# Optimization experiments

Hardware: AMD Instinct MI355X
Metric: run time of the kernel (lower is better)

## Reference

```python
import jax, jax.numpy as jnp
import numpy as np

B, E, N, NREL, K, T, L = 8, 2000, 10000, 25, 16, 3, 32
TAU1 = 10.0

def _clip01(x):
    return jnp.clip(x, 0.0, 1.0)

def setup_inputs():
    key = jax.random.key(0)
    ks = jax.random.split(key, 10)
    ent = jax.random.randint(ks[0], (B,), 0, E)
    input_x = jnp.zeros((B, E), jnp.float32).at[jnp.arange(B), ent].set(1.0)
    tidx = jax.random.randint(ks[1], (E,), 0, K)
    type_mat = jnp.zeros((E, K), jnp.float32).at[jnp.arange(E), tidx].set(1.0)
    heads = jax.random.randint(ks[2], (N,), 0, E)
    tails = jax.random.randint(ks[3], (N,), 0, E)
    rels = jax.random.randint(ks[4], (N,), 0, NREL)
    e2triple = jnp.zeros((E, N), jnp.float32).at[heads, jnp.arange(N)].set(1.0)
    triple2e = jnp.zeros((N, E), jnp.float32).at[jnp.arange(N), tails].set(1.0)
    triple2r = jnp.zeros((N, NREL), jnp.float32).at[jnp.arange(N), rels].set(1.0)
    def ku(k, shape):
        fan_in = int(np.prod(shape[1:]))
        bnd = 1.0 / np.sqrt(fan_in)
        return jax.random.uniform(k, shape, jnp.float32, -bnd, bnd)
    w = ku(ks[5], (T, L, NREL))
    weight = ku(ks[6], (L, 1))
    h = jnp.ones((T, L, NREL - 1), jnp.float32)
    h_x = jnp.ones((L, NREL - 1), jnp.float32)
    h_type = ku(ks[7], (T, L, K))
    h_x_type = ku(ks[8], (L, K))
    alpha = jnp.ones((T, L), jnp.float32)
    beta = jnp.ones((T, L), jnp.float32)
    alpha_x = jnp.ones((L,), jnp.float32)
    beta_x = jnp.ones((L,), jnp.float32)
    return dict(input_x=input_x, type_mat=type_mat, e2triple=e2triple,
                triple2e=triple2e, triple2r=triple2r, w=w, weight=weight,
                h=h, h_x=h_x, h_type=h_type, h_x_type=h_x_type,
                alpha=alpha, beta=beta, alpha_x=alpha_x, beta_x=beta_x, flag=0)

def _forward(input_x, type_mat, e2triple, triple2e, triple2r, w, weight,
             h, h_x, h_type, h_x_type, alpha, beta, alpha_x, beta_x):
    # flag=False, is_training=False path of TCLMModel.forward
    Bb = input_x.shape[0]
    Nn, Ee = triple2e.shape
    Tt, Ll = alpha.shape
    nrel = w.shape[-1]
    half = (nrel - 1) // 2
    x_ori = input_x @ e2triple                      # [B,N]
    e2r = triple2e.T @ triple2r                     # [E,nrel]
    hidden_base = _clip01(e2r)[:, :-1]              # [E,nrel-1]
    hx_raw = _clip01(x_ori @ triple2r)              # [B,nrel]
    hidden_x_base = jnp.concatenate([hx_raw[:, half:-1], hx_raw[:, :half]], axis=-1)
    ax = _clip01(alpha_x / TAU1)
    bx = _clip01(beta_x / TAU1)
    gate_x = 1.0 - _clip01(ax + bx)                 # [L]
    hxp = _clip01(h_x / TAU1)                       # [L,nrel-1]
    hxtp = _clip01(h_x_type / TAU1)                 # [L,K]
    hidden_type_x = input_x @ (type_mat @ hxtp.T)   # [B,L]
    hx_lin = hidden_x_base @ hxp.T                  # [B,L]
    s = None
    for t in range(Tt):
        a = _clip01(alpha[t] / TAU1)                # [L]
        b = _clip01(beta[t] / TAU1)
        hp = _clip01(h[t] / TAU1)                   # [L,nrel-1]
        htp = _clip01(h_type[t] / TAU1)             # [L,K]
        hidden = _clip01(a[None] * (type_mat @ htp.T) + b[None] * (hidden_base @ hp.T))
        hidden = (hidden + (1.0 - _clip01(a + b))[None]).T        # [L,E]
        # note: original code uses alpha/beta (not alpha_x/beta_x) here; replicate
        hidden_x = _clip01(a[None] * hidden_type_x + b[None] * hx_lin) + gate_x[None]  # [B,L]
        w_probs = jax.nn.softmax(w[t], axis=-1)     # [L,nrel]
        srel = triple2r @ w_probs.T                 # [N,L]
        if t == 0:
            sc = x_ori[:, None, :] * srel.T[None]   # [B,L,N]
            s = (sc.reshape(-1, Nn) @ triple2e).reshape(Bb, Ll, Ee)
            s = s * hidden[None] * hidden_x[:, :, None]
        else:
            xprev = (s.reshape(-1, Ee) @ e2triple).reshape(Bb, Ll, Nn)
            sc = xprev * srel.T[None]               # [B,L,N]
            s = (sc.reshape(-1, Nn) @ triple2e).reshape(Bb, Ll, Ee)
            s = s * hidden[None]
    out = jnp.einsum('ble,lk->bek', s, jnp.tanh(weight))[..., 0]  # [B,E]
    return out

def reference(input_x, type_mat, e2triple, triple2e, triple2r, w, weight,
              h, h_x, h_type, h_x_type, alpha, beta, alpha_x, beta_x, flag):
    return _forward(input_x, type_mat, e2triple, triple2e, triple2r, w, weight,
                    h, h_x, h_type, h_x_type, alpha, beta, alpha_x, beta_x)
```

## Files before the change

### kernel.cpp

```cpp
#include <hip/hip_runtime.h>

#define B 8
#define E 2000
#define NTRI 10000
#define NRELS 25
#define KT 16
#define TT 3
#define LL 32
#define TAU1 10.0f
#define XBLK 8192
#define XTHR 256

typedef __attribute__((ext_vector_type(4))) float f32x4;

__device__ __forceinline__ float clip01(float x) { return fminf(fmaxf(x, 0.0f), 1.0f); }

__global__ void __launch_bounds__(XTHR) extract_all(
        const f32x4* __restrict__ e2t, const f32x4* __restrict__ t2e,
        const float4* __restrict__ t2r, const float4* __restrict__ ix,
        const float4* __restrict__ tm,
        int* __restrict__ heads, int* __restrict__ tails, int* __restrict__ rels,
        int* __restrict__ ent, int* __restrict__ tidx, float4* __restrict__ out4) {
    const int gtid = blockIdx.x * XTHR + threadIdx.x;
    const int gs = XBLK * XTHR;

    for (int i = gtid; i < B * E / 4; i += gs) {
        float4 v = ix[i];
        if (v.x != 0.f || v.y != 0.f || v.z != 0.f || v.w != 0.f) {
            int f = i * 4;
            float c[4] = {v.x, v.y, v.z, v.w};
#pragma unroll
            for (int k = 0; k < 4; k++)
                if (c[k] != 0.f) { int a = f + k; int b = a / E; ent[b] = a - b * E; }
        }
    }
    for (int i = gtid; i < E * KT / 4; i += gs) {
        float4 v = tm[i];
        if (v.x != 0.f || v.y != 0.f || v.z != 0.f || v.w != 0.f) {
            int f = i * 4;
            float c[4] = {v.x, v.y, v.z, v.w};
#pragma unroll
            for (int k = 0; k < 4; k++)
                if (c[k] != 0.f) { int a = f + k; int e = a / KT; tidx[e] = a - e * KT; }
        }
    }
    float4 z = make_float4(0.f, 0.f, 0.f, 0.f);
    for (int i = gtid; i < B * E / 4; i += gs) out4[i] = z;

    for (int i = gtid; i < NTRI * NRELS / 4; i += gs) {
        float4 v = t2r[i];
        if (v.x != 0.f || v.y != 0.f || v.z != 0.f || v.w != 0.f) {
            int f = i * 4;
            float c[4] = {v.x, v.y, v.z, v.w};
#pragma unroll
            for (int k = 0; k < 4; k++)
                if (c[k] != 0.f) {
                    int a = f + k;
                    int j = a / NRELS;
                    rels[j] = a - j * NRELS;
                }
        }
    }
    for (int i = gtid; i < E * NTRI / 4; i += gs) {
        f32x4 v = __builtin_nontemporal_load(&e2t[i]);
        if (v.x != 0.f || v.y != 0.f || v.z != 0.f || v.w != 0.f) {
            int f = i * 4;
            float c[4] = {v.x, v.y, v.z, v.w};
#pragma unroll
            for (int k = 0; k < 4; k++)
                if (c[k] != 0.f) {
                    int a = f + k;
                    int head = a / NTRI;
                    heads[a - head * NTRI] = head;
                }
        }
    }
    for (int i = gtid; i < NTRI * E / 4; i += gs) {
        f32x4 v = __builtin_nontemporal_load(&t2e[i]);
        if (v.x != 0.f || v.y != 0.f || v.z != 0.f || v.w != 0.f) {
            int f = i * 4;
            float c[4] = {v.x, v.y, v.z, v.w};
#pragma unroll
            for (int k = 0; k < 4; k++)
                if (c[k] != 0.f) {
                    int a = f + k;
                    int j = a / E;
                    tails[j] = a - j * E;
                }
        }
    }
}

__global__ void __launch_bounds__(512) mega_prop(
        const int* __restrict__ heads, const int* __restrict__ tails,
        const int* __restrict__ rels, const int* __restrict__ ent,
        const int* __restrict__ tidx,
        const float* __restrict__ w, const float* __restrict__ h,
        const float* __restrict__ h_type, const float* __restrict__ alpha,
        const float* __restrict__ beta, const float* __restrict__ h_x,
        const float* __restrict__ h_x_type, const float* __restrict__ alpha_x,
        const float* __restrict__ beta_x, const float* __restrict__ weight,
        float* __restrict__ out) {
    __shared__ float prev[E];
    __shared__ float acc[E];
    __shared__ unsigned int mask_s[E];
    __shared__ int tidx_s[E];
    __shared__ float wrow[NRELS];
    __shared__ float hp[NRELS - 1];
    __shared__ float htpL[KT];
    __shared__ unsigned int relflag;
    __shared__ float extra_s;

    const int NT = 512;
    const int blk = blockIdx.x, b = blk >> 5, l = blk & 31, tid = threadIdx.x;
    const int ent_b = ent[b];

    for (int e = tid; e < E; e += NT) {
        acc[e] = 0.f;
        mask_s[e] = 0u;
        tidx_s[e] = tidx[e];
    }
    if (tid == 0) { relflag = 0u; extra_s = 1.f; }

    const uint4* h4 = (const uint4*)heads;
    const uint4* t4 = (const uint4*)tails;
    const uint4* r4 = (const uint4*)rels;

    for (int t = 0; t < TT; t++) {
        const int tl = t * LL + l;
        if (tid == 0) {
            const float* wr = w + tl * NRELS;
            float mx = wr[0];
            for (int r = 1; r < NRELS; r++) mx = fmaxf(mx, wr[r]);
            float ex[NRELS], s = 0.f;
            for (int r = 0; r < NRELS; r++) { ex[r] = expf(wr[r] - mx); s += ex[r]; }
            float inv = 1.f / s;
            for (int r = 0; r < NRELS; r++) wrow[r] = ex[r] * inv;
        }
        if (tid >= 64 && tid < 64 + NRELS - 1)
            hp[tid - 64] = clip01(h[tl * (NRELS - 1) + (tid - 64)] / TAU1);
        if (tid >= 128 && tid < 128 + KT)
            htpL[tid - 128] = clip01(h_type[tl * KT + (tid - 128)] / TAU1);
        __syncthreads();

        if (t == 0) {
            for (int i = tid; i < NTRI / 4; i += NT) {
                uint4 hh = h4[i], ttv = t4[i], rr = r4[i];
#pragma unroll
                for (int k = 0; k < 4; k++) {
                    unsigned int hd = (k == 0) ? hh.x : (k == 1) ? hh.y : (k == 2) ? hh.z : hh.w;
                    unsigned int ta = (k == 0) ? ttv.x : (k == 1) ? ttv.y : (k == 2) ? ttv.z : ttv.w;
                    unsigned int r  = (k == 0) ? rr.x : (k == 1) ? rr.y : (k == 2) ? rr.z : rr.w;
                    if (r < NRELS - 1) atomicOr(&mask_s[ta], 1u << r);
                    if ((int)hd == ent_b) {
                        atomicAdd(&acc[ta], wrow[r]);
                        atomicOr(&relflag, 1u << r);
                    }
                }
            }
        } else {
            for (int i = tid; i < NTRI / 4; i += NT) {
                uint4 hh = h4[i], ttv = t4[i], rr = r4[i];
#pragma unroll
                for (int k = 0; k < 4; k++) {
                    unsigned int hd = (k == 0) ? hh.x : (k == 1) ? hh.y : (k == 2) ? hh.z : hh.w;
                    float pv = prev[hd];
                    if (pv != 0.f) {
                        unsigned int ta = (k == 0) ? ttv.x : (k == 1) ? ttv.y : (k == 2) ? ttv.z : ttv.w;
                        unsigned int r  = (k == 0) ? rr.x : (k == 1) ? rr.y : (k == 2) ? rr.z : rr.w;
                        atomicAdd(&acc[ta], pv * wrow[r]);
                    }
                }
            }
        }
        __syncthreads();

        const float a = clip01(alpha[tl] / TAU1);
        const float bb = clip01(beta[tl] / TAU1);
        const float base = 1.f - clip01(a + bb);

        if (t == 0 && tid == 0) {
            unsigned int fl = relflag;
            float hxlin = 0.f;
            for (int i = 0; i < NRELS - 1; i++) {
                int pi = (i < 12) ? (12 + i) : (i - 12);
                if ((fl >> pi) & 1u) hxlin += clip01(h_x[l * (NRELS - 1) + i] / TAU1);
            }
            float htx = clip01(h_x_type[l * KT + tidx_s[ent_b]] / TAU1);
            float ax = clip01(alpha_x[l] / TAU1), bx = clip01(beta_x[l] / TAU1);
            extra_s = clip01(a * htx + bb * hxlin) + (1.f - clip01(ax + bx));
        }
        __syncthreads();

        const float extra = (t == 0) ? extra_s : 1.f;

        if (t < TT - 1) {
            for (int e = tid; e < E; e += NT) {
                unsigned int m = mask_s[e];
                float dot = 0.f;
#pragma unroll
                for (int i = 0; i < NRELS - 1; i++) dot += ((m >> i) & 1u) ? hp[i] : 0.f;
                float he = clip01(a * htpL[tidx_s[e]] + bb * dot) + base;
                prev[e] = acc[e] * he * extra;
                acc[e] = 0.f;
            }
        } else {
            float tw = tanhf(weight[l]);
            for (int e = tid; e < E; e += NT) {
                unsigned int m = mask_s[e];
                float dot = 0.f;
#pragma unroll
                for (int i = 0; i < NRELS - 1; i++) dot += ((m >> i) & 1u) ? hp[i] : 0.f;
                float he = clip01(a * htpL[tidx_s[e]] + bb * dot) + base;
                atomicAdd(&out[b * E + e], acc[e] * he * tw);
            }
        }
        __syncthreads();
    }
}

extern "C" void kernel_launch(void* const* d_in, const int* in_sizes, int n_in,
                              void* d_out, int out_size, void* d_ws, size_t ws_size,
                              hipStream_t stream) {
    const float* input_x  = (const float*)d_in[0];
    const float* type_mat = (const float*)d_in[1];
    const float* e2triple = (const float*)d_in[2];
    const float* triple2e = (const float*)d_in[3];
    const float* triple2r = (const float*)d_in[4];
    const float* w        = (const float*)d_in[5];
    const float* weight   = (const float*)d_in[6];
    const float* h        = (const float*)d_in[7];
    const float* h_x      = (const float*)d_in[8];
    const float* h_type   = (const float*)d_in[9];
    const float* h_x_type = (const float*)d_in[10];
    const float* alpha    = (const float*)d_in[11];
    const float* beta     = (const float*)d_in[12];
    const float* alpha_x  = (const float*)d_in[13];
    const float* beta_x   = (const float*)d_in[14];
    (void)in_sizes; (void)n_in; (void)out_size; (void)ws_size;

    char* ws = (char*)d_ws;
    int* heads = (int*)ws;
    int* tails = heads + ((NTRI + 63) & ~63);
    int* rels  = tails + ((NTRI + 63) & ~63);
    int* ent   = rels + ((NTRI + 63) & ~63);
    int* tidx  = ent + 64;

    extract_all<<<XBLK, XTHR, 0, stream>>>((const f32x4*)e2triple, (const f32x4*)triple2e,
                                           (const float4*)triple2r, (const float4*)input_x,
                                           (const float4*)type_mat,
                                           heads, tails, rels, ent, tidx, (float4*)d_out);

    mega_prop<<<B * LL, 512, 0, stream>>>(heads, tails, rels, ent, tidx, w, h, h_type,
                                          alpha, beta, h_x, h_x_type, alpha_x, beta_x,
                                          weight, (float*)d_out);
}
```

Measured before the change: 213.6 us.

## Precompute per-entity relation masks and per-batch head lists in a separate kernel

Adds a build_aux kernel that computes the per-tail relation bitmask once globally and, per batch, a compact list of triples whose head is the query entity. The propagation kernel's first hop now walks only that short list instead of all triples, and the softmax of w moves into the extraction kernel. The extraction kernel also merges the two large dense-matrix scans into one loop, and later hops skip loading tails and relations when all four heads are inactive. The cost is one extra launch, and the lists are capped at LCAP entries, which would silently drop triples if a head had more than that.

```diff
diff --git a/kernel.cpp b/kernel.cpp
--- a/kernel.cpp
+++ b/kernel.cpp
@@ -10,6 +10,7 @@
 #define TAU1 10.0f
 #define XBLK 8192
 #define XTHR 256
+#define LCAP 256
 
 typedef __attribute__((ext_vector_type(4))) float f32x4;
 
@@ -18,75 +19,89 @@
 __global__ void __launch_bounds__(XTHR) extract_all(
         const f32x4* __restrict__ e2t, const f32x4* __restrict__ t2e,
         const float4* __restrict__ t2r, const float4* __restrict__ ix,
-        const float4* __restrict__ tm,
+        const float4* __restrict__ tm, const float* __restrict__ w,
         int* __restrict__ heads, int* __restrict__ tails, int* __restrict__ rels,
-        int* __restrict__ ent, int* __restrict__ tidx, float4* __restrict__ out4) {
+        int* __restrict__ ent, int* __restrict__ tidx,
+        unsigned int* __restrict__ mask_g, int* __restrict__ cnt_g,
+        float* __restrict__ wrow_g, float4* __restrict__ out4) {
     const int gtid = blockIdx.x * XTHR + threadIdx.x;
     const int gs = XBLK * XTHR;
+
+    if (gtid < 2048) mask_g[gtid] = 0u;
+    if (gtid < 64) cnt_g[gtid] = 0;
+    float4 z = make_float4(0.f, 0.f, 0.f, 0.f);
+    for (int i = gtid; i < B * E / 4; i += gs) out4[i] = z;
+
+    if (gtid < TT * LL) {
+        const float* wr = w + gtid * NRELS;
+        float mx = wr[0];
+        for (int r = 1; r < NRELS; r++) mx = fmaxf(mx, wr[r]);
+        float ex[NRELS], s = 0.f;
+        for (int r = 0; r < NRELS; r++) { ex[r] = expf(wr[r] - mx); s += ex[r]; }
+        float inv = 1.f / s;
+        for (int r = 0; r < NRELS; r++) wrow_g[gtid * NRELS + r] = ex[r] * inv;
+    }
 
     for (int i = gtid; i < B * E / 4; i += gs) {
         float4 v = ix[i];
         if (v.x != 0.f || v.y != 0.f || v.z != 0.f || v.w != 0.f) {
-            int f = i * 4;
             float c[4] = {v.x, v.y, v.z, v.w};
 #pragma unroll
             for (int k = 0; k < 4; k++)
-                if (c[k] != 0.f) { int a = f + k; int b = a / E; ent[b] = a - b * E; }
+                if (c[k] != 0.f) { int a = i * 4 + k; int bq = a / E; ent[bq] = a - bq * E; }
         }
     }
     for (int i = gtid; i < E * KT / 4; i += gs) {
         float4 v = tm[i];
         if (v.x != 0.f || v.y != 0.f || v.z != 0.f || v.w != 0.f) {
-            int f = i * 4;
             float c[4] = {v.x, v.y, v.z, v.w};
 #pragma unroll
             for (int k = 0; k < 4; k++)
-                if (c[k] != 0.f) { int a = f + k; int e = a / KT; tidx[e] = a - e * KT; }
-        }
-    }
-    float4 z = make_float4(0.f, 0.f, 0.f, 0.f);
-    for (int i = gtid; i < B * E / 4; i += gs) out4[i] = z;
-
+                if (c[k] != 0.f) { int a = i * 4 + k; int e = a / KT; tidx[e] = a - e * KT; }
+        }
+    }
     for (int i = gtid; i < NTRI * NRELS / 4; i += gs) {
         float4 v = t2r[i];
         if (v.x != 0.f || v.y != 0.f || v.z != 0.f || v.w != 0.f) {
-            int f = i * 4;
             float c[4] = {v.x, v.y, v.z, v.w};
 #pragma unroll
             for (int k = 0; k < 4; k++)
-                if (c[k] != 0.f) {
-                    int a = f + k;
-                    int j = a / NRELS;
-                    rels[j] = a - j * NRELS;
-                }
+                if (c[k] != 0.f) { int a = i * 4 + k; int j = a / NRELS; rels[j] = a - j * NRELS; }
         }
     }
     for (int i = gtid; i < E * NTRI / 4; i += gs) {
-        f32x4 v = __builtin_nontemporal_load(&e2t[i]);
-        if (v.x != 0.f || v.y != 0.f || v.z != 0.f || v.w != 0.f) {
-            int f = i * 4;
-            float c[4] = {v.x, v.y, v.z, v.w};
-#pragma unroll
-            for (int k = 0; k < 4; k++)
-                if (c[k] != 0.f) {
-                    int a = f + k;
-                    int head = a / NTRI;
-                    heads[a - head * NTRI] = head;
-                }
-        }
-    }
-    for (int i = gtid; i < NTRI * E / 4; i += gs) {
-        f32x4 v = __builtin_nontemporal_load(&t2e[i]);
-        if (v.x != 0.f || v.y != 0.f || v.z != 0.f || v.w != 0.f) {
-            int f = i * 4;
-            float c[4] = {v.x, v.y, v.z, v.w};
-#pragma unroll
-            for (int k = 0; k < 4; k++)
-                if (c[k] != 0.f) {
-                    int a = f + k;
-                    int j = a / E;
-                    tails[j] = a - j * E;
-                }
+        f32x4 va = __builtin_nontemporal_load(&e2t[i]);
+        f32x4 vb = __builtin_nontemporal_load(&t2e[i]);
+        if (va.x != 0.f || va.y != 0.f || va.z != 0.f || va.w != 0.f) {
+            float c[4] = {va.x, va.y, va.z, va.w};
+#pragma unroll
+            for (int k = 0; k < 4; k++)
+                if (c[k] != 0.f) { int a = i * 4 + k; int hd = a / NTRI; heads[a - hd * NTRI] = hd; }
+        }
+        if (vb.x != 0.f || vb.y != 0.f || vb.z != 0.f || vb.w != 0.f) {
+            float c[4] = {vb.x, vb.y, vb.z, vb.w};
+#pragma unroll
+            for (int k = 0; k < 4; k++)
+                if (c[k] != 0.f) { int a = i * 4 + k; int j = a / E; tails[j] = a - j * E; }
+        }
+    }
+}
+
+__global__ void __launch_bounds__(256) build_aux(
+        const int* __restrict__ heads, const int* __restrict__ tails,
+        const int* __restrict__ rels, const int* __restrict__ ent,
+        unsigned int* __restrict__ mask_g, int* __restrict__ cnt_g,
+        int* __restrict__ list_g) {
+    int j = blockIdx.x * 256 + threadIdx.x;
+    if (j >= NTRI) return;
+    int r = rels[j];
+    if (r < NRELS - 1) atomicOr(&mask_g[tails[j]], 1u << r);
+    int hd = heads[j];
+#pragma unroll
+    for (int q = 0; q < B; q++) {
+        if (hd == ent[q]) {
+            int p = atomicAdd(&cnt_g[q], 1);
+            if (p < LCAP) list_g[q * LCAP + p] = j;
         }
     }
 }
@@ -95,32 +110,32 @@
         const int* __restrict__ heads, const int* __restrict__ tails,
         const int* __restrict__ rels, const int* __restrict__ ent,
         const int* __restrict__ tidx,
-        const float* __restrict__ w, const float* __restrict__ h,
-        const float* __restrict__ h_type, const float* __restrict__ alpha,
-        const float* __restrict__ beta, const float* __restrict__ h_x,
-        const float* __restrict__ h_x_type, const float* __restrict__ alpha_x,
-        const float* __restrict__ beta_x, const float* __restrict__ weight,
-        float* __restrict__ out) {
-    __shared__ float prev[E];
-    __shared__ float acc[E];
+        const unsigned int* __restrict__ mask_g, const int* __restrict__ cnt_g,
+        const int* __restrict__ list_g, const float* __restrict__ wrow_g,
+        const float* __restrict__ h, const float* __restrict__ h_type,
+        const float* __restrict__ alpha, const float* __restrict__ beta,
+        const float* __restrict__ h_x, const float* __restrict__ h_x_type,
+        const float* __restrict__ alpha_x, const float* __restrict__ beta_x,
+        const float* __restrict__ weight, float* __restrict__ out) {
+    __shared__ float prev_s[E];
+    __shared__ float acc_s[E];
     __shared__ unsigned int mask_s[E];
     __shared__ int tidx_s[E];
-    __shared__ float wrow[NRELS];
-    __shared__ float hp[NRELS - 1];
-    __shared__ float htpL[KT];
-    __shared__ unsigned int relflag;
-    __shared__ float extra_s;
+    __shared__ float wrow_s[NRELS];
+    __shared__ float hp_s[NRELS - 1];
+    __shared__ float htp_s[KT];
+    __shared__ float extra_sh;
 
     const int NT = 512;
-    const int blk = blockIdx.x, b = blk >> 5, l = blk & 31, tid = threadIdx.x;
-    const int ent_b = ent[b];
+    const int bI = blockIdx.x >> 5, l = blockIdx.x & 31, tid = threadIdx.x;
+    const int ent_b = ent[bI];
+    const int cnt = min(cnt_g[bI], LCAP);
 
     for (int e = tid; e < E; e += NT) {
-        acc[e] = 0.f;
-        mask_s[e] = 0u;
+        acc_s[e] = 0.f;
+        mask_s[e] = mask_g[e];
         tidx_s[e] = tidx[e];
     }
-    if (tid == 0) { relflag = 0u; extra_s = 1.f; }
 
     const uint4* h4 = (const uint4*)heads;
     const uint4* t4 = (const uint4*)tails;
@@ -128,48 +143,29 @@
 
     for (int t = 0; t < TT; t++) {
         const int tl = t * LL + l;
-        if (tid == 0) {
-            const float* wr = w + tl * NRELS;
-            float mx = wr[0];
-            for (int r = 1; r < NRELS; r++) mx = fmaxf(mx, wr[r]);
-            float ex[NRELS], s = 0.f;
-            for (int r = 0; r < NRELS; r++) { ex[r] = expf(wr[r] - mx); s += ex[r]; }
-            float inv = 1.f / s;
-            for (int r = 0; r < NRELS; r++) wrow[r] = ex[r] * inv;
-        }
+        if (tid < NRELS) wrow_s[tid] = wrow_g[tl * NRELS + tid];
         if (tid >= 64 && tid < 64 + NRELS - 1)
-            hp[tid - 64] = clip01(h[tl * (NRELS - 1) + (tid - 64)] / TAU1);
+            hp_s[tid - 64] = clip01(h[tl * (NRELS - 1) + (tid - 64)] / TAU1);
         if (tid >= 128 && tid < 128 + KT)
-            htpL[tid - 128] = clip01(h_type[tl * KT + (tid - 128)] / TAU1);
+            htp_s[tid - 128] = clip01(h_type[tl * KT + (tid - 128)] / TAU1);
         __syncthreads();
 
         if (t == 0) {
-            for (int i = tid; i < NTRI / 4; i += NT) {
-                uint4 hh = h4[i], ttv = t4[i], rr = r4[i];
-#pragma unroll
-                for (int k = 0; k < 4; k++) {
-                    unsigned int hd = (k == 0) ? hh.x : (k == 1) ? hh.y : (k == 2) ? hh.z : hh.w;
-                    unsigned int ta = (k == 0) ? ttv.x : (k == 1) ? ttv.y : (k == 2) ? ttv.z : ttv.w;
-                    unsigned int r  = (k == 0) ? rr.x : (k == 1) ? rr.y : (k == 2) ? rr.z : rr.w;
-                    if (r < NRELS - 1) atomicOr(&mask_s[ta], 1u << r);
-                    if ((int)hd == ent_b) {
-                        atomicAdd(&acc[ta], wrow[r]);
-                        atomicOr(&relflag, 1u << r);
-                    }
-                }
+            for (int i = tid; i < cnt; i += NT) {
+                int j = list_g[bI * LCAP + i];
+                atomicAdd(&acc_s[tails[j]], wrow_s[rels[j]]);
             }
         } else {
             for (int i = tid; i < NTRI / 4; i += NT) {
-                uint4 hh = h4[i], ttv = t4[i], rr = r4[i];
-#pragma unroll
-                for (int k = 0; k < 4; k++) {
-                    unsigned int hd = (k == 0) ? hh.x : (k == 1) ? hh.y : (k == 2) ? hh.z : hh.w;
-                    float pv = prev[hd];
-                    if (pv != 0.f) {
-                        unsigned int ta = (k == 0) ? ttv.x : (k == 1) ? ttv.y : (k == 2) ? ttv.z : ttv.w;
-                        unsigned int r  = (k == 0) ? rr.x : (k == 1) ? rr.y : (k == 2) ? rr.z : rr.w;
-                        atomicAdd(&acc[ta], pv * wrow[r]);
-                    }
+                uint4 hh = h4[i];
+                float p0 = prev_s[hh.x], p1 = prev_s[hh.y];
+                float p2 = prev_s[hh.z], p3 = prev_s[hh.w];
+                if (p0 != 0.f || p1 != 0.f || p2 != 0.f || p3 != 0.f) {
+                    uint4 tv = t4[i], rr = r4[i];
+                    if (p0 != 0.f) atomicAdd(&acc_s[tv.x], p0 * wrow_s[rr.x]);
+                    if (p1 != 0.f) atomicAdd(&acc_s[tv.y], p1 * wrow_s[rr.y]);
+                    if (p2 != 0.f) atomicAdd(&acc_s[tv.z], p2 * wrow_s[rr.z]);
+                    if (p3 != 0.f) atomicAdd(&acc_s[tv.w], p3 * wrow_s[rr.w]);
                 }
             }
         }
@@ -180,7 +176,8 @@
         const float base = 1.f - clip01(a + bb);
 
         if (t == 0 && tid == 0) {
-            unsigned int fl = relflag;
+            unsigned int fl = 0u;
+            for (int i = 0; i < cnt; i++) fl |= 1u << rels[list_g[bI * LCAP + i]];
             float hxlin = 0.f;
             for (int i = 0; i < NRELS - 1; i++) {
                 int pi = (i < 12) ? (12 + i) : (i - 12);
@@ -188,21 +185,21 @@
             }
             float htx = clip01(h_x_type[l * KT + tidx_s[ent_b]] / TAU1);
             float ax = clip01(alpha_x[l] / TAU1), bx = clip01(beta_x[l] / TAU1);
-            extra_s = clip01(a * htx + bb * hxlin) + (1.f - clip01(ax + bx));
-        }
-        __syncthreads();
-
-        const float extra = (t == 0) ? extra_s : 1.f;
+            extra_sh = clip01(a * htx + bb * hxlin) + (1.f - clip01(ax + bx));
+        }
+        __syncthreads();
+
+        const float extra = (t == 0) ? extra_sh : 1.f;
 
         if (t < TT - 1) {
             for (int e = tid; e < E; e += NT) {
                 unsigned int m = mask_s[e];
                 float dot = 0.f;
 #pragma unroll
-                for (int i = 0; i < NRELS - 1; i++) dot += ((m >> i) & 1u) ? hp[i] : 0.f;
-                float he = clip01(a * htpL[tidx_s[e]] + bb * dot) + base;
-                prev[e] = acc[e] * he * extra;
-                acc[e] = 0.f;
+                for (int i = 0; i < NRELS - 1; i++) dot += ((m >> i) & 1u) ? hp_s[i] : 0.f;
+                float he = clip01(a * htp_s[tidx_s[e]] + bb * dot) + base;
+                prev_s[e] = acc_s[e] * he * extra;
+                acc_s[e] = 0.f;
             }
         } else {
             float tw = tanhf(weight[l]);
@@ -210,9 +207,9 @@
                 unsigned int m = mask_s[e];
                 float dot = 0.f;
 #pragma unroll
-                for (int i = 0; i < NRELS - 1; i++) dot += ((m >> i) & 1u) ? hp[i] : 0.f;
-                float he = clip01(a * htpL[tidx_s[e]] + bb * dot) + base;
-                atomicAdd(&out[b * E + e], acc[e] * he * tw);
+                for (int i = 0; i < NRELS - 1; i++) dot += ((m >> i) & 1u) ? hp_s[i] : 0.f;
+                float he = clip01(a * htp_s[tidx_s[e]] + bb * dot) + base;
+                atomicAdd(&out[bI * E + e], acc_s[e] * he * tw);
             }
         }
         __syncthreads();
@@ -222,36 +219,43 @@
 extern "C" void kernel_launch(void* const* d_in, const int* in_sizes, int n_in,
                               void* d_out, int out_size, void* d_ws, size_t ws_size,
                               hipStream_t stream) {
-    const float* input_x  = (const float*)d_in[0];
-    const float* type_mat = (const float*)d_in[1];
-    const float* e2triple = (const float*)d_in[2];
-    const float* triple2e = (const float*)d_in[3];
-    const float* triple2r = (const float*)d_in[4];
-    const float* w        = (const float*)d_in[5];
-    const float* weight   = (const float*)d_in[6];
-    const float* h        = (const float*)d_in[7];
-    const float* h_x      = (const float*)d_in[8];
-    const float* h_type   = (const float*)d_in[9];
-    const float* h_x_type = (const float*)d_in[10];
-    const float* alpha    = (const float*)d_in[11];
-    const float* beta     = (const float*)d_in[12];
-    const float* alpha_x  = (const float*)d_in[13];
-    const float* beta_x   = (const float*)d_in[14];
+    const float4* ix       = (const float4*)d_in[0];
+    const float4* tm       = (const float4*)d_in[1];
+    const f32x4*  e2t      = (const f32x4*)d_in[2];
+    const f32x4*  t2e      = (const f32x4*)d_in[3];
+    const float4* t2r      = (const float4*)d_in[4];
+    const float*  w        = (const float*)d_in[5];
+    const float*  weight   = (const float*)d_in[6];
+    const float*  h        = (const float*)d_in[7];
+    const float*  h_x      = (const float*)d_in[8];
+    const float*  h_type   = (const float*)d_in[9];
+    const float*  h_x_type = (const float*)d_in[10];
+    const float*  alpha    = (const float*)d_in[11];
+    const float*  beta     = (const float*)d_in[12];
+    const float*  alpha_x  = (const float*)d_in[13];
+    const float*  beta_x   = (const float*)d_in[14];
     (void)in_sizes; (void)n_in; (void)out_size; (void)ws_size;
 
     char* ws = (char*)d_ws;
     int* heads = (int*)ws;
-    int* tails = heads + ((NTRI + 63) & ~63);
-    int* rels  = tails + ((NTRI + 63) & ~63);
-    int* ent   = rels + ((NTRI + 63) & ~63);
+    int* tails = heads + 10048;
+    int* rels  = tails + 10048;
+    int* ent   = rels + 10048;
     int* tidx  = ent + 64;
-
-    extract_all<<<XBLK, XTHR, 0, stream>>>((const f32x4*)e2triple, (const f32x4*)triple2e,
-                                           (const float4*)triple2r, (const float4*)input_x,
-                                           (const float4*)type_mat,
-                                           heads, tails, rels, ent, tidx, (float4*)d_out);
-
-    mega_prop<<<B * LL, 512, 0, stream>>>(heads, tails, rels, ent, tidx, w, h, h_type,
-                                          alpha, beta, h_x, h_x_type, alpha_x, beta_x,
-                                          weight, (float*)d_out);
-}
+    unsigned int* mask_g = (unsigned int*)(tidx + 2048);
+    int* cnt_g = (int*)(mask_g + 2048);
+    int* list_g = cnt_g + 64;
+    float* wrow_g = (float*)(list_g + B * LCAP);
+
+    extract_all<<<XBLK, XTHR, 0, stream>>>(e2t, t2e, t2r, ix, tm, w,
+                                           heads, tails, rels, ent, tidx,
+                                           mask_g, cnt_g, wrow_g, (float4*)d_out);
+
+    build_aux<<<(NTRI + 255) / 256, 256, 0, stream>>>(heads, tails, rels, ent,
+                                                      mask_g, cnt_g, list_g);
+
+    mega_prop<<<B * LL, 512, 0, stream>>>(heads, tails, rels, ent, tidx,
+                                          mask_g, cnt_g, list_g, wrow_g,
+                                          h, h_type, alpha, beta, h_x, h_x_type,
+                                          alpha_x, beta_x, weight, (float*)d_out);
+}
```

Result: no change. 212.3 us (-0.6%).
